# Performance work log

Measured on AMD Instinct MI355X. Metric: run time of the kernel, lower is better.

The kernel has to match this reference:

```python
import jax, jax.numpy as jnp
import numpy as np

D_MODEL = 512
NUM_HEADS = 8
QUERY_GROUPS = 2
HEAD_DIM = D_MODEL // NUM_HEADS  # 64
ROPE_THETA = 10000.0
SCALE = 0.125  # 1/sqrt(head_dim)
NEG_INF = -1e9


def setup_inputs() -> dict:
    key = jax.random.key(0)
    k1, k2, k3 = jax.random.split(key, 3)
    B, T, S = 2, 512, 16
    x = jax.random.normal(k1, (B, T, S, D_MODEL), jnp.float32)
    padding_mask = jnp.ones((B, T * S), jnp.int32)  # [B, T*H*W], all valid
    qkv_dim = NUM_HEADS * HEAD_DIM + 2 * QUERY_GROUPS * HEAD_DIM  # 768
    qkv_w = jax.random.normal(k2, (qkv_dim, D_MODEL), jnp.float32) / np.float32(np.sqrt(D_MODEL))
    o_w = jax.random.normal(k3, (D_MODEL, NUM_HEADS * HEAD_DIM), jnp.float32) / np.float32(np.sqrt(D_MODEL))
    return {"x": x, "padding_mask": padding_mask, "qkv_w": qkv_w, "o_w": o_w}


def _rope(v, pos):
    # v: [N, T, h, d]; classic RoPE (rotate-half) over temporal positions
    half = v.shape[-1] // 2
    inv_freq = 1.0 / (ROPE_THETA ** (jnp.arange(0, half, dtype=jnp.float32) / half))
    ang = pos[:, None] * inv_freq  # [T, half]
    cos = jnp.cos(ang)[None, :, None, :]
    sin = jnp.sin(ang)[None, :, None, :]
    v1, v2 = v[..., :half], v[..., half:]
    return jnp.concatenate([v1 * cos - v2 * sin, v1 * sin + v2 * cos], axis=-1)


def reference(x, padding_mask, qkv_w, o_w):
    B, T, S, D = x.shape
    # temporal attention: flatten spatial patches into batch -> [B*S, T, D]
    xt = x.transpose(0, 2, 1, 3).reshape(B * S, T, D)
    qkv = xt @ qkv_w.T  # [B*S, T, (H+2G)*hd]
    q_end = NUM_HEADS * HEAD_DIM
    k_end = q_end + QUERY_GROUPS * HEAD_DIM
    q = qkv[..., :q_end].reshape(B * S, T, NUM_HEADS, HEAD_DIM)
    k = qkv[..., q_end:k_end].reshape(B * S, T, QUERY_GROUPS, HEAD_DIM)
    v = qkv[..., k_end:].reshape(B * S, T, QUERY_GROUPS, HEAD_DIM)
    pos = jnp.arange(T, dtype=jnp.float32)
    q = _rope(q, pos)
    k = _rope(k, pos)
    # GQA: broadcast each KV group to its query heads
    rep = NUM_HEADS // QUERY_GROUPS
    k = jnp.repeat(k, rep, axis=2)
    v = jnp.repeat(v, rep, axis=2)
    scores = jnp.einsum('nqhd,nkhd->nhqk', q, k) * SCALE  # [B*S, H, T, T]
    causal = jnp.tril(jnp.ones((T, T), bool))
    pm = padding_mask.astype(bool).reshape(-1, T)  # [B*S, T] query-side mask (as in torch path)
    mask = causal[None, None, :, :] & pm[:, None, :, None]
    scores = jnp.where(mask, scores, NEG_INF)
    attn = jax.nn.softmax(scores, axis=-1)
    out = jnp.einsum('nhqk,nkhd->nqhd', attn, v).reshape(B * S, T, D)
    out = out @ o_w.T  # output projection
    return out.reshape(B, S, T, D).transpose(0, 2, 1, 3)  # back to [B, T, S, D]
```

## Files before the change

kernel.cpp:

```cpp
#include <hip/hip_runtime.h>
#include <hip/hip_bf16.h>

typedef __attribute__((ext_vector_type(8))) short bf16x8;
typedef __attribute__((ext_vector_type(4))) float f32x4;
typedef __attribute__((ext_vector_type(4))) short s16x4;

#define DM 512
#define T_SEQ 512
#define NSEQ 32
#define MROWS 16384
#define QKV_DIM 768
#define HD 64
#define NEG_INF_F (-1000000000.0f)
#define LOG2E 1.44269504088896340736f

__device__ __forceinline__ short f2bf(float f) {
    unsigned int u = __builtin_bit_cast(unsigned int, f);
    unsigned int r = (u + 0x7FFFu + ((u >> 16) & 1u)) >> 16;
    return (short)r;
}

__device__ __forceinline__ short f2bf_hw(float f) {
    __hip_bfloat16 h = __float2bfloat16(f);
    return __builtin_bit_cast(short, h);
}

__device__ __forceinline__ void gload16(const void* g, void* l) {
    __builtin_amdgcn_global_load_lds(
        (const __attribute__((address_space(1))) void*)g,
        (__attribute__((address_space(3))) void*)l, 16, 0, 0);
}

__global__ __launch_bounds__(128) void k_convert(
    const float* __restrict__ x, const float* __restrict__ qkvw, const float* __restrict__ owf,
    short* __restrict__ xt, short* __restrict__ qw, short* __restrict__ ow,
    float* __restrict__ cosT, float* __restrict__ sinT)
{
    int bidx = blockIdx.x, tid = threadIdx.x;
    if (bidx < MROWS) {
        int m = bidx; int n = m >> 9, t = m & 511, b = n >> 4, s = n & 15;
        const float* src = x + ((size_t)((b * 512 + t) * 16 + s)) * 512;
        float4 v = *(const float4*)(src + tid * 4);
        s16x4 o; o.x = f2bf(v.x); o.y = f2bf(v.y); o.z = f2bf(v.z); o.w = f2bf(v.w);
        *(s16x4*)(xt + (size_t)m * 512 + tid * 4) = o;
    } else if (bidx < MROWS + 1280) {
        int wr = bidx - MROWS;
        const float* src; short* dst;
        if (wr < QKV_DIM) { src = qkvw + (size_t)wr * 512; dst = qw + (size_t)wr * 512; }
        else             { src = owf + (size_t)(wr - QKV_DIM) * 512; dst = ow + (size_t)(wr - QKV_DIM) * 512; }
        float4 v = *(const float4*)(src + tid * 4);
        s16x4 o; o.x = f2bf(v.x); o.y = f2bf(v.y); o.z = f2bf(v.z); o.w = f2bf(v.w);
        *(s16x4*)(dst + tid * 4) = o;
    } else {
        int idx = (bidx - (MROWS + 1280)) * 128 + tid;
        int t = idx >> 5, d = idx & 31;
        float inv = powf(10000.0f, -(float)d * (1.0f / 32.0f));
        float ang = (float)t * inv;
        float sv, cv; sincosf(ang, &sv, &cv);
        cosT[idx] = cv; sinT[idx] = sv;
    }
}

__device__ __forceinline__ void gemm_mainloop(
    const short* __restrict__ Ab, const short* __restrict__ Bb, int K,
    short* As, short* Bs, int wave, int lane, f32x4 acc[4][4])
{
    int wr = (wave >> 1) * 64, wc = (wave & 1) * 64;
    for (int kt = 0; kt < K; kt += 32) {
        __syncthreads();
        #pragma unroll
        for (int c = 0; c < 2; ++c) {
            int chunk = (wave * 2 + c) * 64 + lane;
            int row = chunk >> 2, kc = chunk & 3;
            gload16(Ab + (size_t)row * K + kt + kc * 8, As + (wave * 2 + c) * 512);
            gload16(Bb + (size_t)row * K + kt + kc * 8, Bs + (wave * 2 + c) * 512);
        }
        __syncthreads();
        bf16x8 af[4], bg[4];
        #pragma unroll
        for (int mf = 0; mf < 4; ++mf)
            af[mf] = *(const bf16x8*)(As + (wr + mf * 16 + (lane & 15)) * 32 + ((lane >> 4) << 3));
        #pragma unroll
        for (int nf = 0; nf < 4; ++nf)
            bg[nf] = *(const bf16x8*)(Bs + (wc + nf * 16 + (lane & 15)) * 32 + ((lane >> 4) << 3));
        #pragma unroll
        for (int mf = 0; mf < 4; ++mf)
            #pragma unroll
            for (int nf = 0; nf < 4; ++nf)
                acc[mf][nf] = __builtin_amdgcn_mfma_f32_16x16x32_bf16(af[mf], bg[nf], acc[mf][nf], 0, 0, 0);
    }
}

__global__ __launch_bounds__(256) void k_gemm_qkv(
    const short* __restrict__ xt, const short* __restrict__ qw,
    const float* __restrict__ cosT, const float* __restrict__ sinT,
    short* __restrict__ qb, short* __restrict__ kb, short* __restrict__ vtb)
{
    __shared__ short As[128 * 32], Bs[128 * 32];
    int tid = threadIdx.x, wave = tid >> 6, lane = tid & 63;
    int bm = blockIdx.x, bn = blockIdx.y;
    f32x4 acc[4][4] = {};
    gemm_mainloop(xt + (size_t)bm * 128 * 512, qw + (size_t)bn * 128 * 512, 512, As, Bs, wave, lane, acc);

    const float QSC = 0.125f * LOG2E;
    int wr = (wave >> 1) * 64, wc = (wave & 1) * 64;
    int gbase = bn * 128 + wc;
    int cl = lane & 15;
    #pragma unroll
    for (int mf = 0; mf < 4; ++mf) {
        #pragma unroll
        for (int rg = 0; rg < 4; ++rg) {
            int r = bm * 128 + wr + mf * 16 + ((lane >> 4) << 2) + rg;
            int n = r >> 9, t = r & 511;
            #pragma unroll
            for (int nf = 0; nf < 2; ++nf) {
                int dlo = nf * 16 + cl;
                float v1 = acc[mf][nf][rg];
                float v2 = acc[mf][nf + 2][rg];
                if (gbase < 512) {
                    int h = gbase >> 6;
                    float c = cosT[t * 32 + dlo], s = sinT[t * 32 + dlo];
                    size_t base = ((size_t)(n * 8 + h) * 512 + t) * 64;
                    qb[base + dlo]      = f2bf((v1 * c - v2 * s) * QSC);
                    qb[base + dlo + 32] = f2bf((v1 * s + v2 * c) * QSC);
                } else if (gbase < 640) {
                    int g = (gbase - 512) >> 6;
                    float c = cosT[t * 32 + dlo], s = sinT[t * 32 + dlo];
                    size_t base = ((size_t)(n * 2 + g) * 512 + t) * 64;
                    kb[base + dlo]      = f2bf(v1 * c - v2 * s);
                    kb[base + dlo + 32] = f2bf(v1 * s + v2 * c);
                } else {
                    int g = (gbase - 640) >> 6;
                    size_t base = ((size_t)(n * 2 + g) * 64) * 512;
                    vtb[base + (size_t)dlo * 512 + t]        = f2bf(v1);
                    vtb[base + (size_t)(dlo + 32) * 512 + t] = f2bf(v2);
                }
            }
        }
    }
}

__global__ __launch_bounds__(256) void k_attn(
    const short* __restrict__ qb, const short* __restrict__ kb, const short* __restrict__ vtb,
    const int* __restrict__ pm, short* __restrict__ ao)
{
    __shared__ short Kt[2][64 * 64];
    __shared__ short Vt[2][64 * 64];
    __shared__ short Pws[4][16 * 64];
    int tid = threadIdx.x, wave = tid >> 6, lane = tid & 63;
    int cl = lane & 15, g = lane >> 4;
    int bid = blockIdx.x;
    int c = bid & 3, h = (bid >> 2) & 7, n = bid >> 5;
    int kg = h >> 2;
    const short* Qb = qb + ((size_t)(n * 8 + h) * 512) * 64;
    const short* Kb = kb + ((size_t)(n * 2 + kg) * 512) * 64;
    const short* Vb = vtb + ((size_t)(n * 2 + kg) * 64) * 512;

    auto stage = [&](int jt, int buf) {
        int c0 = jt * 64;
        #pragma unroll
        for (int cc = 0; cc < 2; ++cc) {
            int chunk = (wave * 2 + cc) * 64 + lane;
            int row = chunk >> 3, kc = chunk & 7;
            int sw = (kc ^ (row & 7)) << 3;
            gload16(Kb + (size_t)(c0 + row) * 64 + sw, &Kt[buf][(wave * 2 + cc) * 512]);
            gload16(Vb + (size_t)row * 512 + c0 + sw, &Vt[buf][(wave * 2 + cc) * 512]);
        }
    };

    stage(0, 0);
    int buf = 0;
    #pragma unroll
    for (int ph = 0; ph < 2; ++ph) {
        int rowb = (ph ? (7 - c) : c) * 64 + wave * 16;
        int NTp = ph ? (8 - c) : (c + 1);
        bf16x8 qf[2];
        #pragma unroll
        for (int ks = 0; ks < 2; ++ks)
            qf[ks] = *(const bf16x8*)(Qb + (size_t)(rowb + cl) * 64 + ks * 32 + (g << 3));
        f32x4 Oc[4] = {};
        float mrow = -1e30f, lrow = 0.f;
        bool rv = pm[n * 512 + rowb + cl] != 0;
        int rq = rowb + cl;

        for (int jt = 0; jt < NTp; ++jt) {
            __syncthreads();
            if (jt + 1 < NTp) stage(jt + 1, buf ^ 1);
            else if (ph == 0) stage(0, buf ^ 1);
            int c0 = jt * 64;
            const short* Kc = Kt[buf];
            const short* Vc = Vt[buf];
            buf ^= 1;

            f32x4 sacc[4] = {};
            #pragma unroll
            for (int ks = 0; ks < 2; ++ks) {
                #pragma unroll
                for (int nf = 0; nf < 4; ++nf) {
                    int row = nf * 16 + cl;
                    int kc = ks * 4 + g;
                    bf16x8 kf = *(const bf16x8*)(Kc + row * 64 + ((kc ^ (row & 7)) << 3));
                    sacc[nf] = __builtin_amdgcn_mfma_f32_16x16x32_bf16(kf, qf[ks], sacc[nf], 0, 0, 0);
                }
            }

            const bool diag = (jt == NTp - 1);
            float rmax = -1e30f;
            if (diag) {
                #pragma unroll
                for (int nf = 0; nf < 4; ++nf)
                    #pragma unroll
                    for (int rg = 0; rg < 4; ++rg) {
                        int kv = c0 + nf * 16 + g * 4 + rg;
                        float sv = sacc[nf][rg];
                        sv = (kv <= rq && rv) ? sv : NEG_INF_F;
                        sacc[nf][rg] = sv;
                        rmax = fmaxf(rmax, sv);
                    }
            } else {
                #pragma unroll
                for (int nf = 0; nf < 4; ++nf)
                    #pragma unroll
                    for (int rg = 0; rg < 4; ++rg)
                        rmax = fmaxf(rmax, sacc[nf][rg]);
            }
            rmax = fmaxf(rmax, __shfl_xor(rmax, 16));
            rmax = fmaxf(rmax, __shfl_xor(rmax, 32));
            float mold = mrow;
            int defer = __all(rmax - mold <= 8.0f);
            float mnew = defer ? mold : fmaxf(mold, rmax);
            mrow = mnew;
            float rsum = 0.f;
            #pragma unroll
            for (int nf = 0; nf < 4; ++nf) {
                s16x4 pk;
                #pragma unroll
                for (int rg = 0; rg < 4; ++rg) {
                    float p = exp2f(sacc[nf][rg] - mnew);
                    rsum += p;
                    ((short*)&pk)[rg] = f2bf_hw(p);
                }
                *(s16x4*)(&Pws[wave][cl * 64 + ((((nf << 1) + (g >> 1)) ^ (cl & 7)) << 3) + ((g & 1) << 2)]) = pk;
            }
            rsum += __shfl_xor(rsum, 16);
            rsum += __shfl_xor(rsum, 32);
            if (defer) {
                lrow += rsum;
            } else {
                float alpha = exp2f(mold - mnew);
                lrow = lrow * alpha + rsum;
                #pragma unroll
                for (int rg = 0; rg < 4; ++rg) {
                    float av = __shfl(alpha, (lane & 48) + (g << 2) + rg);
                    #pragma unroll
                    for (int nf = 0; nf < 4; ++nf) Oc[nf][rg] *= av;
                }
            }

            #pragma unroll
            for (int ks = 0; ks < 2; ++ks) {
                bf16x8 pf = *(const bf16x8*)(&Pws[wave][cl * 64 + (((ks * 4 + g) ^ (cl & 7)) << 3)]);
                #pragma unroll
                for (int nf = 0; nf < 4; ++nf) {
                    int row = nf * 16 + cl;
                    int kc = ks * 4 + g;
                    bf16x8 vf = *(const bf16x8*)(Vc + row * 64 + ((kc ^ (row & 7)) << 3));
                    Oc[nf] = __builtin_amdgcn_mfma_f32_16x16x32_bf16(pf, vf, Oc[nf], 0, 0, 0);
                }
            }
        }

        #pragma unroll
        for (int rg = 0; rg < 4; ++rg) {
            float li = __shfl(lrow, (lane & 48) + (g << 2) + rg);
            float inv = 1.0f / li;
            int r = rowb + g * 4 + rg;
            size_t base = ((size_t)n * 512 + r) * 512 + h * 64;
            #pragma unroll
            for (int nf = 0; nf < 4; ++nf)
                ao[base + nf * 16 + cl] = f2bf_hw(Oc[nf][rg] * inv);
        }
    }
}

__global__ __launch_bounds__(256) void k_gemm_out(
    const short* __restrict__ ao, const short* __restrict__ ow, float* __restrict__ out)
{
    __shared__ short As[128 * 32], Bs[128 * 32];
    int tid = threadIdx.x, wave = tid >> 6, lane = tid & 63;
    int bm = blockIdx.x, bn = blockIdx.y;
    f32x4 acc[4][4] = {};
    gemm_mainloop(ao + (size_t)bm * 128 * 512, ow + (size_t)bn * 128 * 512, 512, As, Bs, wave, lane, acc);

    int wr = (wave >> 1) * 64, wc = (wave & 1) * 64;
    #pragma unroll
    for (int mf = 0; mf < 4; ++mf) {
        #pragma unroll
        for (int rg = 0; rg < 4; ++rg) {
            int r = bm * 128 + wr + mf * 16 + ((lane >> 4) << 2) + rg;
            int n = r >> 9, t = r & 511, b = n >> 4, s = n & 15;
            size_t obase = ((size_t)((b * 512 + t) * 16 + s)) * 512;
            #pragma unroll
            for (int nf = 0; nf < 4; ++nf) {
                int ccc = bn * 128 + wc + nf * 16 + (lane & 15);
                out[obase + ccc] = acc[mf][nf][rg];
            }
        }
    }
}

extern "C" void kernel_launch(void* const* d_in, const int* in_sizes, int n_in,
                              void* d_out, int out_size, void* d_ws, size_t ws_size,
                              hipStream_t stream) {
    (void)in_sizes; (void)n_in; (void)out_size; (void)ws_size;
    const float* x    = (const float*)d_in[0];
    const int*   pmsk = (const int*)d_in[1];
    const float* qkvw = (const float*)d_in[2];
    const float* owf  = (const float*)d_in[3];
    char* ws = (char*)d_ws;
    short* xt   = (short*)(ws + 0);
    short* qw   = (short*)(ws + 16777216);
    short* ow   = (short*)(ws + 17563648);
    float* cosT = (float*)(ws + 18087936);
    float* sinT = (float*)(ws + 18153472);
    short* qbuf = (short*)(ws + 18219008);
    short* kbuf = (short*)(ws + 34996224);
    short* vtbuf= (short*)(ws + 39190528);
    short* aobuf = xt;
    float* out = (float*)d_out;

    k_convert<<<dim3(17792), dim3(128), 0, stream>>>(x, qkvw, owf, xt, qw, ow, cosT, sinT);
    k_gemm_qkv<<<dim3(128, 6), dim3(256), 0, stream>>>(xt, qw, cosT, sinT, qbuf, kbuf, vtbuf);
    k_attn<<<dim3(1024), dim3(256), 0, stream>>>(qbuf, kbuf, vtbuf, pmsk, aobuf);
    k_gemm_out<<<dim3(128, 4), dim3(256), 0, stream>>>(aobuf, ow, out);
}
```

Measured before the change: 90.13 us.

## Double-buffer GEMM LDS tiles and stage V transpose through shared memory

The GEMM main loop now uses two LDS buffers, issuing the next K-tile's global-to-LDS loads before computing on the current tile, so load latency can overlap MFMA work and one barrier per iteration goes away. The V-projection epilogue transposes each 16x64 fragment through a per-wave LDS scratch and writes 16-byte vectors to the transposed V buffer instead of scattered 2-byte stores. The rounding conversion switches to the hardware bf16 intrinsic. LDS use per block doubles, which may reduce occupancy.

```diff
diff --git a/kernel.cpp b/kernel.cpp
--- a/kernel.cpp
+++ b/kernel.cpp
@@ -61,13 +61,14 @@
     }
 }
 
-__device__ __forceinline__ void gemm_mainloop(
+__device__ __forceinline__ void gemm_mainloop_db(
     const short* __restrict__ Ab, const short* __restrict__ Bb, int K,
-    short* As, short* Bs, int wave, int lane, f32x4 acc[4][4])
+    short* As0, short* As1, short* Bs0, short* Bs1,
+    int wave, int lane, f32x4 acc[4][4])
 {
     int wr = (wave >> 1) * 64, wc = (wave & 1) * 64;
-    for (int kt = 0; kt < K; kt += 32) {
-        __syncthreads();
+    int cl = lane & 15, g = lane >> 4;
+    auto stg = [&](int kt, short* As, short* Bs) {
         #pragma unroll
         for (int c = 0; c < 2; ++c) {
             int chunk = (wave * 2 + c) * 64 + lane;
@@ -75,14 +76,22 @@
             gload16(Ab + (size_t)row * K + kt + kc * 8, As + (wave * 2 + c) * 512);
             gload16(Bb + (size_t)row * K + kt + kc * 8, Bs + (wave * 2 + c) * 512);
         }
+    };
+    stg(0, As0, Bs0);
+    for (int kt = 0; kt < K; kt += 32) {
+        short* Asc = (kt & 32) ? As1 : As0;
+        short* Bsc = (kt & 32) ? Bs1 : Bs0;
+        short* Asn = (kt & 32) ? As0 : As1;
+        short* Bsn = (kt & 32) ? Bs0 : Bs1;
         __syncthreads();
+        if (kt + 32 < K) stg(kt + 32, Asn, Bsn);
         bf16x8 af[4], bg[4];
         #pragma unroll
         for (int mf = 0; mf < 4; ++mf)
-            af[mf] = *(const bf16x8*)(As + (wr + mf * 16 + (lane & 15)) * 32 + ((lane >> 4) << 3));
+            af[mf] = *(const bf16x8*)(Asc + (wr + mf * 16 + cl) * 32 + (g << 3));
         #pragma unroll
         for (int nf = 0; nf < 4; ++nf)
-            bg[nf] = *(const bf16x8*)(Bs + (wc + nf * 16 + (lane & 15)) * 32 + ((lane >> 4) << 3));
+            bg[nf] = *(const bf16x8*)(Bsc + (wc + nf * 16 + cl) * 32 + (g << 3));
         #pragma unroll
         for (int mf = 0; mf < 4; ++mf)
             #pragma unroll
@@ -96,46 +105,69 @@
     const float* __restrict__ cosT, const float* __restrict__ sinT,
     short* __restrict__ qb, short* __restrict__ kb, short* __restrict__ vtb)
 {
-    __shared__ short As[128 * 32], Bs[128 * 32];
+    __shared__ short As0[128 * 32], As1[128 * 32], Bs0[128 * 32], Bs1[128 * 32];
+    __shared__ short Vld[4][16 * 64];
     int tid = threadIdx.x, wave = tid >> 6, lane = tid & 63;
+    int cl = lane & 15, g = lane >> 4;
     int bm = blockIdx.x, bn = blockIdx.y;
     f32x4 acc[4][4] = {};
-    gemm_mainloop(xt + (size_t)bm * 128 * 512, qw + (size_t)bn * 128 * 512, 512, As, Bs, wave, lane, acc);
+    gemm_mainloop_db(xt + (size_t)bm * 128 * 512, qw + (size_t)bn * 128 * 512, 512,
+                     As0, As1, Bs0, Bs1, wave, lane, acc);
 
     const float QSC = 0.125f * LOG2E;
     int wr = (wave >> 1) * 64, wc = (wave & 1) * 64;
     int gbase = bn * 128 + wc;
-    int cl = lane & 15;
-    #pragma unroll
-    for (int mf = 0; mf < 4; ++mf) {
-        #pragma unroll
-        for (int rg = 0; rg < 4; ++rg) {
-            int r = bm * 128 + wr + mf * 16 + ((lane >> 4) << 2) + rg;
-            int n = r >> 9, t = r & 511;
+
+    if (gbase < 640) {
+        #pragma unroll
+        for (int mf = 0; mf < 4; ++mf) {
+            #pragma unroll
+            for (int rg = 0; rg < 4; ++rg) {
+                int r = bm * 128 + wr + mf * 16 + (g << 2) + rg;
+                int n = r >> 9, t = r & 511;
+                #pragma unroll
+                for (int nf = 0; nf < 2; ++nf) {
+                    int dlo = nf * 16 + cl;
+                    float v1 = acc[mf][nf][rg];
+                    float v2 = acc[mf][nf + 2][rg];
+                    float c = cosT[t * 32 + dlo], s = sinT[t * 32 + dlo];
+                    if (gbase < 512) {
+                        int h = gbase >> 6;
+                        size_t base = ((size_t)(n * 8 + h) * 512 + t) * 64;
+                        qb[base + dlo]      = f2bf_hw((v1 * c - v2 * s) * QSC);
+                        qb[base + dlo + 32] = f2bf_hw((v1 * s + v2 * c) * QSC);
+                    } else {
+                        int gk = (gbase - 512) >> 6;
+                        size_t base = ((size_t)(n * 2 + gk) * 512 + t) * 64;
+                        kb[base + dlo]      = f2bf_hw(v1 * c - v2 * s);
+                        kb[base + dlo + 32] = f2bf_hw(v1 * s + v2 * c);
+                    }
+                }
+            }
+        }
+    } else {
+        int gq = (gbase - 640) >> 6;
+        #pragma unroll
+        for (int mf = 0; mf < 4; ++mf) {
             #pragma unroll
             for (int nf = 0; nf < 2; ++nf) {
                 int dlo = nf * 16 + cl;
-                float v1 = acc[mf][nf][rg];
-                float v2 = acc[mf][nf + 2][rg];
-                if (gbase < 512) {
-                    int h = gbase >> 6;
-                    float c = cosT[t * 32 + dlo], s = sinT[t * 32 + dlo];
-                    size_t base = ((size_t)(n * 8 + h) * 512 + t) * 64;
-                    qb[base + dlo]      = f2bf((v1 * c - v2 * s) * QSC);
-                    qb[base + dlo + 32] = f2bf((v1 * s + v2 * c) * QSC);
-                } else if (gbase < 640) {
-                    int g = (gbase - 512) >> 6;
-                    float c = cosT[t * 32 + dlo], s = sinT[t * 32 + dlo];
-                    size_t base = ((size_t)(n * 2 + g) * 512 + t) * 64;
-                    kb[base + dlo]      = f2bf(v1 * c - v2 * s);
-                    kb[base + dlo + 32] = f2bf(v1 * s + v2 * c);
-                } else {
-                    int g = (gbase - 640) >> 6;
-                    size_t base = ((size_t)(n * 2 + g) * 64) * 512;
-                    vtb[base + (size_t)dlo * 512 + t]        = f2bf(v1);
-                    vtb[base + (size_t)(dlo + 32) * 512 + t] = f2bf(v2);
-                }
-            }
+                s16x4 plo, phi;
+                #pragma unroll
+                for (int rg = 0; rg < 4; ++rg) {
+                    ((short*)&plo)[rg] = f2bf_hw(acc[mf][nf][rg]);
+                    ((short*)&phi)[rg] = f2bf_hw(acc[mf][nf + 2][rg]);
+                }
+                *(s16x4*)(&Vld[wave][dlo * 16 + (g << 2)])        = plo;
+                *(s16x4*)(&Vld[wave][(dlo + 32) * 16 + (g << 2)]) = phi;
+            }
+            int r0 = bm * 128 + wr + mf * 16;
+            int n = r0 >> 9, t0 = r0 & 511;
+            size_t vb = ((size_t)(n * 2 + gq) * 64 + lane) * 512;
+            bf16x8 va = *(const bf16x8*)(&Vld[wave][lane * 16]);
+            bf16x8 vb8 = *(const bf16x8*)(&Vld[wave][lane * 16 + 8]);
+            *(bf16x8*)(vtb + vb + t0)     = va;
+            *(bf16x8*)(vtb + vb + t0 + 8) = vb8;
         }
     }
 }
@@ -286,11 +318,12 @@
 __global__ __launch_bounds__(256) void k_gemm_out(
     const short* __restrict__ ao, const short* __restrict__ ow, float* __restrict__ out)
 {
-    __shared__ short As[128 * 32], Bs[128 * 32];
+    __shared__ short As0[128 * 32], As1[128 * 32], Bs0[128 * 32], Bs1[128 * 32];
     int tid = threadIdx.x, wave = tid >> 6, lane = tid & 63;
     int bm = blockIdx.x, bn = blockIdx.y;
     f32x4 acc[4][4] = {};
-    gemm_mainloop(ao + (size_t)bm * 128 * 512, ow + (size_t)bn * 128 * 512, 512, As, Bs, wave, lane, acc);
+    gemm_mainloop_db(ao + (size_t)bm * 128 * 512, ow + (size_t)bn * 128 * 512, 512,
+                     As0, As1, Bs0, Bs1, wave, lane, acc);
 
     int wr = (wave >> 1) * 64, wc = (wave & 1) * 64;
     #pragma unroll
```

Result: faster. 84.30 us (median of 2 runs) (-6.5%).
